# Optimization experiments

Hardware: AMD Instinct MI355X
Metric: run time of the kernel (lower is better)

Reference implementation:

```python
import jax, jax.numpy as jnp
import numpy as np

N_NODES = 100000
N_EDGES = 1600000
IN_CH = 128
HID = 256
OUT_CH = 128
N_GRAPHS = 2048


def setup_inputs() -> dict:
    key = jax.random.key(0)
    ks = jax.random.split(key, 12)
    x = jax.random.normal(ks[0], (N_NODES, IN_CH), dtype=jnp.float32)
    edge_index = jax.random.randint(ks[1], (2, N_EDGES), 0, N_NODES, dtype=jnp.int32)
    batch = jnp.sort(jax.random.randint(ks[2], (N_NODES,), 0, N_GRAPHS, dtype=jnp.int32))
    s = lambda k, shp, fan: jax.random.normal(k, shp, dtype=jnp.float32) / np.sqrt(fan)
    params = {
        # SAGEConv1: lin_l (applied to aggregated neighbors, has bias) and lin_r (root)
        "W1l": s(ks[3], (IN_CH, HID), IN_CH), "b1": jnp.zeros((HID,), jnp.float32),
        "W1r": s(ks[4], (IN_CH, HID), IN_CH),
        # SAGEConv2
        "W2l": s(ks[5], (HID, HID), HID), "b2": jnp.zeros((HID,), jnp.float32),
        "W2r": s(ks[6], (HID, HID), HID),
        # MLP head
        "W3": s(ks[7], (HID, HID), HID), "b3": jnp.zeros((HID,), jnp.float32),
        "W4": s(ks[8], (HID, OUT_CH), HID), "b4": jnp.zeros((OUT_CH,), jnp.float32),
    }
    return {"x": x, "edge_index": edge_index, "batch": batch, **params}


def _sage_conv(x, src, dst, Wl, bl, Wr, num_nodes):
    # PyG SAGEConv (aggr='mean'): out_i = Wl @ mean_{j->i} x_j + bl + Wr @ x_i
    agg = jax.ops.segment_sum(x[src], dst, num_segments=num_nodes)  # [N, C]
    cnt = jax.ops.segment_sum(jnp.ones((src.shape[0],), x.dtype), dst, num_segments=num_nodes)
    mean = agg / jnp.maximum(cnt, 1.0)[:, None]
    return mean @ Wl + bl + x @ Wr


def reference(x, edge_index, batch, W1l, b1, W1r, W2l, b2, W2r, W3, b3, W4, b4):
    src, dst = edge_index[0], edge_index[1]
    h = jax.nn.relu(_sage_conv(x, src, dst, W1l, b1, W1r, N_NODES))
    # dropout is identity in eval mode
    h = jax.nn.relu(_sage_conv(h, src, dst, W2l, b2, W2r, N_NODES))
    # global_mean_pool over graphs
    psum = jax.ops.segment_sum(h, batch, num_segments=N_GRAPHS)  # [G, HID]
    gcnt = jax.ops.segment_sum(jnp.ones((h.shape[0],), h.dtype), batch, num_segments=N_GRAPHS)
    pooled = psum / jnp.maximum(gcnt, 1.0)[:, None]
    # MLP head
    hidden = jax.nn.relu(pooled @ W3 + b3)
    return hidden @ W4 + b4  # [G, OUT_CH]
```

## Files before the change

kernel.cpp:

```cpp
#include <hip/hip_runtime.h>

#define N_NODES 100000
#define N_EDGES 1600000
#define IN_CH 128
#define HID 256
#define OUT_CH 128
#define N_GRAPHS 2048

#define NBUK 391
#define CHUNK 8192

typedef __attribute__((ext_vector_type(8))) short bf16x8;
typedef __attribute__((ext_vector_type(4))) float f32x4;
typedef __attribute__((ext_vector_type(2))) float f32x2;

__device__ inline unsigned short f2b(float f) {
    unsigned int u = __builtin_bit_cast(unsigned int, f);
    u = (u + 0x7FFF + ((u >> 16) & 1)) >> 16;
    return (unsigned short)u;
}
__device__ inline float b2f(unsigned short h) {
    unsigned int u = (unsigned int)h << 16;
    return __builtin_bit_cast(float, u);
}

#define GLOAD_LDS16(gsrc, ldst)                                                   \
    __builtin_amdgcn_global_load_lds(                                             \
        (const __attribute__((address_space(1))) void*)(gsrc),                    \
        (__attribute__((address_space(3))) void*)(ldst), 16, 0, 0)

#define SCAN_ITEMS 8
#define SCAN_TILE (256 * SCAN_ITEMS)

__global__ void scan1_k(const int* __restrict__ in, int* __restrict__ out,
                        int* __restrict__ bsums, int n) {
    __shared__ int wsum[4];
    int base = blockIdx.x * SCAN_TILE + (int)threadIdx.x * SCAN_ITEMS;
    int v[SCAN_ITEMS];
    int s = 0;
    #pragma unroll
    for (int i = 0; i < SCAN_ITEMS; ++i) {
        v[i] = (base + i < n) ? in[base + i] : 0;
        s += v[i];
    }
    int lane = threadIdx.x & 63, wid = threadIdx.x >> 6;
    int incl = s;
    #pragma unroll
    for (int off = 1; off < 64; off <<= 1) {
        int t = __shfl_up(incl, off, 64);
        if (lane >= off) incl += t;
    }
    if (lane == 63) wsum[wid] = incl;
    __syncthreads();
    int wprefix = 0;
    #pragma unroll
    for (int w = 0; w < 4; ++w)
        if (w < wid) wprefix += wsum[w];
    int run = wprefix + incl - s;
    #pragma unroll
    for (int i = 0; i < SCAN_ITEMS; ++i) {
        if (base + i < n) out[base + i] = run;
        run += v[i];
    }
    if (threadIdx.x == 255) bsums[blockIdx.x] = wprefix + incl;
}

__global__ void scan2_k(int* __restrict__ bsums, int nb, int* __restrict__ total) {
    __shared__ int wsum[4];
    int v = ((int)threadIdx.x < nb) ? bsums[threadIdx.x] : 0;
    int lane = threadIdx.x & 63, wid = threadIdx.x >> 6;
    int incl = v;
    #pragma unroll
    for (int off = 1; off < 64; off <<= 1) {
        int t = __shfl_up(incl, off, 64);
        if (lane >= off) incl += t;
    }
    if (lane == 63) wsum[wid] = incl;
    __syncthreads();
    int wprefix = 0;
    #pragma unroll
    for (int w = 0; w < 4; ++w)
        if (w < wid) wprefix += wsum[w];
    if ((int)threadIdx.x < nb) bsums[threadIdx.x] = wprefix + incl - v;
    if (threadIdx.x == 255) *total = wprefix + incl;
}

__global__ void bucket_count_k(const int* __restrict__ dst, int* __restrict__ bcnt, int E) {
    __shared__ int cnt[NBUK];
    int tid = threadIdx.x;
    for (int i = tid; i < NBUK; i += 256) cnt[i] = 0;
    __syncthreads();
    int e0 = blockIdx.x * CHUNK;
    int eend = min(e0 + CHUNK, E);
    for (int e = e0 + tid; e < eend; e += 256)
        atomicAdd(&cnt[dst[e] >> 8], 1);
    __syncthreads();
    for (int i = tid; i < NBUK; i += 256)
        if (cnt[i]) atomicAdd(&bcnt[i], cnt[i]);
}

__global__ void bin_scatter_k(const int* __restrict__ src, const int* __restrict__ dst,
                              const int* __restrict__ bbase, int* __restrict__ bcur,
                              uint2* __restrict__ staging, int E) {
    __shared__ int cnt[NBUK];
    __shared__ int gbase[NBUK];
    int tid = threadIdx.x;
    for (int i = tid; i < NBUK; i += 256) cnt[i] = 0;
    __syncthreads();
    int e0 = blockIdx.x * CHUNK;
    int eend = min(e0 + CHUNK, E);
    for (int e = e0 + tid; e < eend; e += 256)
        atomicAdd(&cnt[dst[e] >> 8], 1);
    __syncthreads();
    for (int i = tid; i < NBUK; i += 256) {
        int c = cnt[i];
        gbase[i] = c ? (bbase[i] + atomicAdd(&bcur[i], c)) : 0;
        cnt[i] = 0;
    }
    __syncthreads();
    for (int e = e0 + tid; e < eend; e += 256) {
        int d = dst[e];
        int b = d >> 8;
        int l = atomicAdd(&cnt[b], 1);
        uint2 p; p.x = (unsigned)src[e]; p.y = (unsigned)d;
        staging[(size_t)gbase[b] + l] = p;
    }
}

__global__ void csr_build_k(const uint2* __restrict__ staging, const int* __restrict__ bbase,
                            int* __restrict__ row_ofs, int* __restrict__ csr) {
    __shared__ int ldeg[256];
    __shared__ int lofs[256];
    __shared__ int wsum[4];
    int b = blockIdx.x, tid = threadIdx.x;
    int base = bbase[b];
    int cnt = bbase[b + 1] - base;
    ldeg[tid] = 0;
    __syncthreads();
    const uint2* sp = staging + base;
    for (int i = tid; i < cnt; i += 256)
        atomicAdd(&ldeg[sp[i].y & 255], 1);
    __syncthreads();
    int v = ldeg[tid];
    int lane = tid & 63, wid = tid >> 6;
    int incl = v;
    #pragma unroll
    for (int off = 1; off < 64; off <<= 1) {
        int t = __shfl_up(incl, off, 64);
        if (lane >= off) incl += t;
    }
    if (lane == 63) wsum[wid] = incl;
    __syncthreads();
    int wprefix = 0;
    #pragma unroll
    for (int w = 0; w < 4; ++w)
        if (w < wid) wprefix += wsum[w];
    int excl = wprefix + incl - v;
    lofs[tid] = excl;
    int node = b * 256 + tid;
    if (node < N_NODES) row_ofs[node] = base + excl;
    if (b == NBUK - 1 && tid == 0) row_ofs[N_NODES] = N_EDGES;
    ldeg[tid] = 0;
    __syncthreads();
    for (int i = tid; i < cnt; i += 256) {
        uint2 p = sp[i];
        int d = (int)p.y & 255;
        int pos = atomicAdd(&ldeg[d], 1);
        csr[base + lofs[d] + pos] = (int)p.x;
    }
}

__global__ void gofs_search_k(const int* __restrict__ batch, int* __restrict__ gofs,
                              int n, int G) {
    int g = blockIdx.x * blockDim.x + threadIdx.x;
    if (g > G) return;
    if (g == G) { gofs[G] = n; return; }
    int lo = 0, hi = n;
    while (lo < hi) {
        int mid = (lo + hi) >> 1;
        if (batch[mid] < g) lo = mid + 1; else hi = mid;
    }
    gofs[g] = lo;
}

__global__ void wt_concat_k(const float* __restrict__ Wl, const float* __restrict__ Wr,
                            unsigned short* __restrict__ out, int K1, int K2, int N) {
    int idx = blockIdx.x * blockDim.x + threadIdx.x;
    int KT = K1 + K2;
    if (idx >= N * KT) return;
    int n = idx / KT, k = idx % KT;
    float v = (k < K1) ? Wl[(size_t)k * N + n] : Wr[(size_t)(k - K1) * N + n];
    out[idx] = f2b(v);
}

__global__ void f2b8_k(const float* __restrict__ in, unsigned short* __restrict__ outb,
                       unsigned char* __restrict__ out8, size_t n8) {
    size_t i = (size_t)blockIdx.x * blockDim.x + threadIdx.x;
    if (i >= n8) return;
    float4 a = ((const float4*)in)[i * 2];
    float4 b = ((const float4*)in)[i * 2 + 1];
    unsigned short ob[8];
    ob[0] = f2b(a.x); ob[1] = f2b(a.y); ob[2] = f2b(a.z); ob[3] = f2b(a.w);
    ob[4] = f2b(b.x); ob[5] = f2b(b.y); ob[6] = f2b(b.z); ob[7] = f2b(b.w);
    ((uint4*)outb)[i] = *(const uint4*)ob;
    int w0 = 0, w1 = 0;
    w0 = __builtin_amdgcn_cvt_pk_fp8_f32(a.x, a.y, w0, false);
    w0 = __builtin_amdgcn_cvt_pk_fp8_f32(a.z, a.w, w0, true);
    w1 = __builtin_amdgcn_cvt_pk_fp8_f32(b.x, b.y, w1, false);
    w1 = __builtin_amdgcn_cvt_pk_fp8_f32(b.z, b.w, w1, true);
    uint2 o8; o8.x = (unsigned int)w0; o8.y = (unsigned int)w1;
    ((uint2*)out8)[i] = o8;
}

template <int C>
__global__ void agg_f8_k(const unsigned char* __restrict__ X8, const int* __restrict__ row_ofs,
                         const int* __restrict__ csr, unsigned short* __restrict__ out, int n) {
    constexpr int GL = C / 16;
    constexpr int NG = 64 / GL;
    int w = (int)((blockIdx.x * blockDim.x + threadIdx.x) >> 6);
    int lane = threadIdx.x & 63;
    if (w >= n) return;
    int g = lane / GL, il = lane % GL;
    int s = row_ofs[w], e = row_ofs[w + 1];
    float a[16];
    #pragma unroll
    for (int t = 0; t < 16; ++t) a[t] = 0.f;

    int j = s + g;
    for (; j + NG < e; j += 2 * NG) {
        int i0 = csr[j], i1 = csr[j + NG];
        uint4 r0 = *(const uint4*)&X8[(size_t)i0 * C + il * 16];
        uint4 r1 = *(const uint4*)&X8[(size_t)i1 * C + il * 16];
        const unsigned int* q0 = (const unsigned int*)&r0;
        const unsigned int* q1 = (const unsigned int*)&r1;
        #pragma unroll
        for (int t = 0; t < 4; ++t) {
            f32x2 lo = __builtin_amdgcn_cvt_pk_f32_fp8(q0[t], false);
            f32x2 hi = __builtin_amdgcn_cvt_pk_f32_fp8(q0[t], true);
            a[t * 4 + 0] += lo.x; a[t * 4 + 1] += lo.y;
            a[t * 4 + 2] += hi.x; a[t * 4 + 3] += hi.y;
        }
        #pragma unroll
        for (int t = 0; t < 4; ++t) {
            f32x2 lo = __builtin_amdgcn_cvt_pk_f32_fp8(q1[t], false);
            f32x2 hi = __builtin_amdgcn_cvt_pk_f32_fp8(q1[t], true);
            a[t * 4 + 0] += lo.x; a[t * 4 + 1] += lo.y;
            a[t * 4 + 2] += hi.x; a[t * 4 + 3] += hi.y;
        }
    }
    if (j < e) {
        int i0 = csr[j];
        uint4 r0 = *(const uint4*)&X8[(size_t)i0 * C + il * 16];
        const unsigned int* q0 = (const unsigned int*)&r0;
        #pragma unroll
        for (int t = 0; t < 4; ++t) {
            f32x2 lo = __builtin_amdgcn_cvt_pk_f32_fp8(q0[t], false);
            f32x2 hi = __builtin_amdgcn_cvt_pk_f32_fp8(q0[t], true);
            a[t * 4 + 0] += lo.x; a[t * 4 + 1] += lo.y;
            a[t * 4 + 2] += hi.x; a[t * 4 + 3] += hi.y;
        }
    }

    #pragma unroll
    for (int m = GL; m < 64; m <<= 1)
        #pragma unroll
        for (int t = 0; t < 16; ++t) a[t] += __shfl_xor(a[t], m, 64);

    if (g == 0) {
        float inv = 1.0f / (float)max(e - s, 1);
        uint4 o0, o1;
        unsigned short* p0 = (unsigned short*)&o0;
        unsigned short* p1 = (unsigned short*)&o1;
        #pragma unroll
        for (int t = 0; t < 8; ++t) p0[t] = f2b(a[t] * inv);
        #pragma unroll
        for (int t = 0; t < 8; ++t) p1[t] = f2b(a[8 + t] * inv);
        *(uint4*)&out[(size_t)w * C + il * 16] = o0;
        *(uint4*)&out[(size_t)w * C + il * 16 + 8] = o1;
    }
}

__global__ void pool_mean_k(const unsigned short* __restrict__ H, const int* __restrict__ gofs,
                            float* __restrict__ pooled, int G) {
    int g = (int)((blockIdx.x * blockDim.x + threadIdx.x) >> 6);
    int lane = threadIdx.x & 63;
    if (g >= G) return;
    int s = gofs[g], e = gofs[g + 1];
    float a0 = 0.f, a1 = 0.f, a2 = 0.f, a3 = 0.f;
    for (int r = s; r < e; ++r) {
        ushort4 t = ((const ushort4*)(H + (size_t)r * HID))[lane];
        a0 += b2f(t.x); a1 += b2f(t.y); a2 += b2f(t.z); a3 += b2f(t.w);
    }
    float inv = 1.0f / (float)max(e - s, 1);
    float4 o; o.x = a0 * inv; o.y = a1 * inv; o.z = a2 * inv; o.w = a3 * inv;
    ((float4*)(pooled + (size_t)g * HID))[lane] = o;
}

__launch_bounds__(256)
__global__ void mfma_gemm_k(const unsigned short* __restrict__ A1, int K1,
                            const unsigned short* __restrict__ A2, int K2,
                            const unsigned short* __restrict__ Bt,
                            const float* __restrict__ bias, int M, int Nfull,
                            void* __restrict__ Cptr, unsigned char* __restrict__ f8out,
                            int c_bf16, int do_relu) {
    __shared__ short ldsA[3 * 4096];
    __shared__ short ldsB[3 * 4096];
    int tid = threadIdx.x, lane = tid & 63;
    int wid = tid >> 6, wm = wid >> 1, wn = wid & 1;
    int row0 = blockIdx.x * 128, col0 = blockIdx.y * 128;
    int q = lane >> 4, l15 = lane & 15;
    int KT = K1 + K2;
    int nk = KT / 32;

    int rr = tid >> 2;
    int c8 = ((tid & 3) ^ (rr & 3)) * 8;
    int dof = wid * 512;

    auto stage = [&](int t, short* bA, short* bB) {
        int kt = t * 32;
        const unsigned short* Asrc; int kk, Ks;
        if (kt < K1) { Asrc = A1; kk = kt; Ks = K1; }
        else         { Asrc = A2; kk = kt - K1; Ks = K2; }
        #pragma unroll
        for (int h = 0; h < 2; ++h) {
            int r = h * 64 + rr;
            int gr = min(row0 + r, M - 1);
            GLOAD_LDS16(Asrc + (size_t)gr * Ks + kk + c8, bA + h * 2048 + dof);
            GLOAD_LDS16(Bt + (size_t)(col0 + r) * KT + kt + c8, bB + h * 2048 + dof);
        }
    };

    f32x4 acc[4][4] = {};

    stage(0, ldsA, ldsB);
    stage(1, ldsA + 4096, ldsB + 4096);
    stage(2, ldsA + 8192, ldsB + 8192);

    int bi = 0;
    for (int t = 0; t < nk; ++t) {
        if (t + 2 < nk)      asm volatile("s_waitcnt vmcnt(8)" ::: "memory");
        else if (t + 1 < nk) asm volatile("s_waitcnt vmcnt(4)" ::: "memory");
        else                 asm volatile("s_waitcnt vmcnt(0)" ::: "memory");
        asm volatile("s_barrier" ::: "memory");

        short* bA = ldsA + bi * 4096;
        short* bB = ldsB + bi * 4096;
        bf16x8 af[4], bfr[4];
        #pragma unroll
        for (int i = 0; i < 4; ++i) {
            int r = wm * 64 + i * 16 + l15;
            af[i] = *(const bf16x8*)&bA[r * 32 + (q ^ (r & 3)) * 8];
        }
        #pragma unroll
        for (int j = 0; j < 4; ++j) {
            int r = wn * 64 + j * 16 + l15;
            bfr[j] = *(const bf16x8*)&bB[r * 32 + (q ^ (r & 3)) * 8];
        }
        #pragma unroll
        for (int i = 0; i < 4; ++i)
            #pragma unroll
            for (int j = 0; j < 4; ++j)
                acc[i][j] = __builtin_amdgcn_mfma_f32_16x16x32_bf16(af[i], bfr[j], acc[i][j], 0, 0, 0);

        asm volatile("s_barrier" ::: "memory");
        if (t + 3 < nk) stage(t + 3, bA, bB);
        bi = (bi == 2) ? 0 : bi + 1;
    }

    #pragma unroll
    for (int i = 0; i < 4; ++i) {
        #pragma unroll
        for (int reg = 0; reg < 4; ++reg) {
            int r = row0 + wm * 64 + i * 16 + q * 4 + reg;
            if (r < M) {
                #pragma unroll
                for (int j = 0; j < 4; ++j) {
                    int cc = col0 + wn * 64 + j * 16 + l15;
                    float v = acc[i][j][reg] + bias[cc];
                    if (do_relu) v = fmaxf(v, 0.f);
                    if (c_bf16) ((unsigned short*)Cptr)[(size_t)r * Nfull + cc] = f2b(v);
                    else        ((float*)Cptr)[(size_t)r * Nfull + cc] = v;
                    if (f8out) {
                        int w8 = __builtin_amdgcn_cvt_pk_fp8_f32(v, v, 0, false);
                        f8out[(size_t)r * Nfull + cc] = (unsigned char)(w8 & 0xFF);
                    }
                }
            }
        }
    }
}

#define BM_ 64
#define BK_ 16

template <int BN_>
__launch_bounds__(256)
__global__ void gemm2_k(const float* __restrict__ A1, const float* __restrict__ B1, int K1,
                        const float* __restrict__ bias, float* __restrict__ C,
                        int M, int N, int do_relu) {
    constexpr int TCOLS = BN_ / 8;
    constexpr int TROWS = 256 / TCOLS;
    constexpr int TM = BM_ / TROWS;
    __shared__ float As[BK_][BM_ + 4];
    __shared__ float Bs[BK_][BN_ + 4];
    int tid = threadIdx.x;
    int row0 = blockIdx.x * BM_;
    int col0 = blockIdx.y * BN_;
    int tx = tid % TCOLS, ty = tid / TCOLS;

    float acc[TM][8];
    #pragma unroll
    for (int i = 0; i < TM; ++i)
        #pragma unroll
        for (int j = 0; j < 8; ++j) acc[i][j] = 0.f;

    int ar = tid >> 2;
    int ak = (tid & 3) * 4;

    for (int kt = 0; kt < K1; kt += BK_) {
        {
            int r = row0 + ar;
            int rc = min(r, M - 1);
            float4 v = *(const float4*)(A1 + (size_t)rc * K1 + kt + ak);
            As[ak + 0][ar] = v.x;
            As[ak + 1][ar] = v.y;
            As[ak + 2][ar] = v.z;
            As[ak + 3][ar] = v.w;
        }
        {
            #pragma unroll
            for (int h = 0; h < BN_ / 64; ++h) {
                int idx = h * 256 + tid;
                int kr = idx / (BN_ / 4);
                int c4 = idx % (BN_ / 4);
                float4 v = *(const float4*)(B1 + (size_t)(kt + kr) * N + col0 + c4 * 4);
                *(float4*)&Bs[kr][c4 * 4] = v;
            }
        }
        __syncthreads();

        #pragma unroll
        for (int k = 0; k < BK_; ++k) {
            float a[TM], b[8];
            #pragma unroll
            for (int v = 0; v < TM / 4; ++v)
                *(float4*)&a[v * 4] = *(const float4*)&As[k][ty * TM + v * 4];
            *(float4*)&b[0] = *(const float4*)&Bs[k][tx * 8];
            *(float4*)&b[4] = *(const float4*)&Bs[k][tx * 8 + 4];
            #pragma unroll
            for (int i = 0; i < TM; ++i)
                #pragma unroll
                for (int j = 0; j < 8; ++j) acc[i][j] = fmaf(a[i], b[j], acc[i][j]);
        }
        __syncthreads();
    }

    float bv[8];
    #pragma unroll
    for (int j = 0; j < 8; ++j) bv[j] = bias[col0 + tx * 8 + j];
    #pragma unroll
    for (int i = 0; i < TM; ++i) {
        int r = row0 + ty * TM + i;
        if (r < M) {
            float* cp = C + (size_t)r * N + col0 + tx * 8;
            float o[8];
            #pragma unroll
            for (int j = 0; j < 8; ++j) {
                float v = acc[i][j] + bv[j];
                o[j] = do_relu ? fmaxf(v, 0.f) : v;
            }
            *(float4*)(cp + 0) = *(float4*)&o[0];
            *(float4*)(cp + 4) = *(float4*)&o[4];
        }
    }
}

extern "C" void kernel_launch(void* const* d_in, const int* in_sizes, int n_in,
                              void* d_out, int out_size, void* d_ws, size_t ws_size,
                              hipStream_t stream) {
    const float* x    = (const float*)d_in[0];
    const int*   ei   = (const int*)d_in[1];
    const int*   batch= (const int*)d_in[2];
    const float* W1l  = (const float*)d_in[3];
    const float* b1   = (const float*)d_in[4];
    const float* W1r  = (const float*)d_in[5];
    const float* W2l  = (const float*)d_in[6];
    const float* b2   = (const float*)d_in[7];
    const float* W2r  = (const float*)d_in[8];
    const float* W3   = (const float*)d_in[9];
    const float* b3   = (const float*)d_in[10];
    const float* W4   = (const float*)d_in[11];
    const float* b4   = (const float*)d_in[12];
    float* out = (float*)d_out;

    const int N = N_NODES, E = N_EDGES, G = N_GRAPHS;
    const int* src = ei;
    const int* dst = ei + E;

    char* ws = (char*)d_ws;
    size_t off = 0;
    auto alloc = [&](size_t bytes) -> char* {
        off = (off + 255) & ~(size_t)255;
        char* p = ws + off;
        off += bytes;
        return p;
    };
    int* bcnt    = (int*)alloc((size_t)NBUK * 4);
    int* bcur    = (int*)alloc((size_t)NBUK * 4);
    size_t zero_span = (size_t)((char*)(bcur + NBUK) - (char*)bcnt);
    int* bbase   = (int*)alloc((size_t)(NBUK + 1) * 4);
    int* bsums   = (int*)alloc(256 * 4);
    int* row_ofs = (int*)alloc((size_t)(N + 1) * 4);
    int* gofs    = (int*)alloc((size_t)(G + 1) * 4);
    uint2* staging = (uint2*)alloc((size_t)E * 8);
    int* csr     = (int*)alloc((size_t)E * 4);
    unsigned short* xb    = (unsigned short*)alloc((size_t)N * IN_CH * 2);
    unsigned short* mean1 = (unsigned short*)alloc((size_t)N * IN_CH * 2);
    unsigned short* h1    = (unsigned short*)alloc((size_t)N * HID * 2);
    unsigned short* mean2 = (unsigned short*)alloc((size_t)N * HID * 2);
    unsigned short* h2    = xb;
    unsigned char*  x8    = (unsigned char*)alloc((size_t)N * IN_CH);
    unsigned char*  h1f8  = (unsigned char*)alloc((size_t)N * HID);
    unsigned short* W1T   = (unsigned short*)alloc((size_t)HID * (IN_CH + IN_CH) * 2);
    unsigned short* W2T   = (unsigned short*)alloc((size_t)HID * (HID + HID) * 2);
    float* pooled = (float*)alloc((size_t)G * HID * 4);
    float* hidden = (float*)alloc((size_t)G * HID * 4);
    (void)ws_size;

    hipMemsetAsync(bcnt, 0, zero_span, stream);

    const int EB = (E + CHUNK - 1) / CHUNK;
    bucket_count_k<<<EB, 256, 0, stream>>>(dst, bcnt, E);
    scan1_k<<<1, 256, 0, stream>>>(bcnt, bbase, bsums, NBUK);
    scan2_k<<<1, 256, 0, stream>>>(bsums, 1, bbase + NBUK);
    bin_scatter_k<<<EB, 256, 0, stream>>>(src, dst, bbase, bcur, staging, E);
    csr_build_k<<<NBUK, 256, 0, stream>>>(staging, bbase, row_ofs, csr);

    gofs_search_k<<<(G + 256) / 256, 256, 0, stream>>>(batch, gofs, N, G);

    wt_concat_k<<<(HID * 2 * IN_CH + 255) / 256, 256, 0, stream>>>(W1l, W1r, W1T, IN_CH, IN_CH, HID);
    wt_concat_k<<<(HID * 2 * HID + 255) / 256, 256, 0, stream>>>(W2l, W2r, W2T, HID, HID, HID);
    f2b8_k<<<(int)(((size_t)N * IN_CH / 8 + 255) / 256), 256, 0, stream>>>(
        x, xb, x8, (size_t)N * IN_CH / 8);

    const int MB = (N + 127) / 128;

    agg_f8_k<IN_CH><<<(N + 3) / 4, 256, 0, stream>>>(x8, row_ofs, csr, mean1, N);
    mfma_gemm_k<<<dim3(MB, HID / 128), 256, 0, stream>>>(
        mean1, IN_CH, xb, IN_CH, W1T, b1, N, HID, h1, h1f8, 1, 1);

    agg_f8_k<HID><<<(N + 3) / 4, 256, 0, stream>>>(h1f8, row_ofs, csr, mean2, N);
    mfma_gemm_k<<<dim3(MB, HID / 128), 256, 0, stream>>>(
        mean2, HID, h1, HID, W2T, b2, N, HID, h2, nullptr, 1, 1);

    pool_mean_k<<<(G + 3) / 4, 256, 0, stream>>>(h2, gofs, pooled, G);

    gemm2_k<HID><<<dim3(G / BM_, 1), 256, 0, stream>>>(
        pooled, W3, HID, b3, hidden, G, HID, 1);
    gemm2_k<OUT_CH><<<dim3(G / BM_, 1), 256, 0, stream>>>(
        hidden, W4, HID, b4, out, G, OUT_CH, 0);
}
```

Before: 551.7 us.

## Widen MFMA GEMM tile to 128x256 with 8 waves and split-stage pipeline

```diff
diff --git a/kernel.cpp b/kernel.cpp
--- a/kernel.cpp
+++ b/kernel.cpp
@@ -296,75 +296,114 @@
     ((float4*)(pooled + (size_t)g * HID))[lane] = o;
 }
 
-__launch_bounds__(256)
+__launch_bounds__(512)
 __global__ void mfma_gemm_k(const unsigned short* __restrict__ A1, int K1,
                             const unsigned short* __restrict__ A2, int K2,
                             const unsigned short* __restrict__ Bt,
                             const float* __restrict__ bias, int M, int Nfull,
                             void* __restrict__ Cptr, unsigned char* __restrict__ f8out,
                             int c_bf16, int do_relu) {
-    __shared__ short ldsA[3 * 4096];
-    __shared__ short ldsB[3 * 4096];
+    __shared__ short lds[3 * 24576];
     int tid = threadIdx.x, lane = tid & 63;
-    int wid = tid >> 6, wm = wid >> 1, wn = wid & 1;
-    int row0 = blockIdx.x * 128, col0 = blockIdx.y * 128;
+    int wid = tid >> 6, wm = wid >> 2, wn = wid & 3;
+    int row0 = blockIdx.x * 128, col0 = blockIdx.y * 256;
     int q = lane >> 4, l15 = lane & 15;
     int KT = K1 + K2;
-    int nk = KT / 32;
-
-    int rr = tid >> 2;
-    int c8 = ((tid & 3) ^ (rr & 3)) * 8;
-    int dof = wid * 512;
-
-    auto stage = [&](int t, short* bA, short* bB) {
-        int kt = t * 32;
+    int nk = KT / 64;
+
+    int lr = lane >> 3;
+    int cg = (lane & 7) ^ lr;
+
+    auto stagep = [&](int t, int part) {
+        int kt = t * 64;
         const unsigned short* Asrc; int kk, Ks;
         if (kt < K1) { Asrc = A1; kk = kt; Ks = K1; }
         else         { Asrc = A2; kk = kt - K1; Ks = K2; }
-        #pragma unroll
-        for (int h = 0; h < 2; ++h) {
-            int r = h * 64 + rr;
-            int gr = min(row0 + r, M - 1);
-            GLOAD_LDS16(Asrc + (size_t)gr * Ks + kk + c8, bA + h * 2048 + dof);
-            GLOAD_LDS16(Bt + (size_t)(col0 + r) * KT + kt + c8, bB + h * 2048 + dof);
+        short* bufA = lds + (t % 3) * 24576;
+        short* bufB = bufA + 8192;
+        if (part == 0) {
+            #pragma unroll
+            for (int h = 0; h < 2; ++h) {
+                int rl = h * 64 + wid * 8 + lr;
+                int gr = min(row0 + rl, M - 1);
+                GLOAD_LDS16(Asrc + (size_t)gr * Ks + kk + cg * 8,
+                            bufA + (h * 64 + wid * 8) * 64);
+            }
+            {
+                int rl = wid * 8 + lr;
+                GLOAD_LDS16(Bt + (size_t)(col0 + rl) * KT + kt + cg * 8,
+                            bufB + (wid * 8) * 64);
+            }
+        } else {
+            #pragma unroll
+            for (int h = 1; h < 4; ++h) {
+                int rl = h * 64 + wid * 8 + lr;
+                GLOAD_LDS16(Bt + (size_t)(col0 + rl) * KT + kt + cg * 8,
+                            bufB + (h * 64 + wid * 8) * 64);
+            }
         }
     };
 
     f32x4 acc[4][4] = {};
 
-    stage(0, ldsA, ldsB);
-    stage(1, ldsA + 4096, ldsB + 4096);
-    stage(2, ldsA + 8192, ldsB + 8192);
-
-    int bi = 0;
+    stagep(0, 0); stagep(0, 1);
+    stagep(1, 0); stagep(1, 1);
+
     for (int t = 0; t < nk; ++t) {
-        if (t + 2 < nk)      asm volatile("s_waitcnt vmcnt(8)" ::: "memory");
-        else if (t + 1 < nk) asm volatile("s_waitcnt vmcnt(4)" ::: "memory");
-        else                 asm volatile("s_waitcnt vmcnt(0)" ::: "memory");
+        if (t + 1 < nk) asm volatile("s_waitcnt vmcnt(6)" ::: "memory");
+        else            asm volatile("s_waitcnt vmcnt(0)" ::: "memory");
         asm volatile("s_barrier" ::: "memory");
-
-        short* bA = ldsA + bi * 4096;
-        short* bB = ldsB + bi * 4096;
-        bf16x8 af[4], bfr[4];
-        #pragma unroll
-        for (int i = 0; i < 4; ++i) {
-            int r = wm * 64 + i * 16 + l15;
-            af[i] = *(const bf16x8*)&bA[r * 32 + (q ^ (r & 3)) * 8];
-        }
-        #pragma unroll
-        for (int j = 0; j < 4; ++j) {
-            int r = wn * 64 + j * 16 + l15;
-            bfr[j] = *(const bf16x8*)&bB[r * 32 + (q ^ (r & 3)) * 8];
-        }
-        #pragma unroll
-        for (int i = 0; i < 4; ++i)
+        const short* bufA = lds + (t % 3) * 24576;
+        const short* bufB = bufA + 8192;
+
+        bf16x8 bfr[4][2], af[2][2];
+        #pragma unroll
+        for (int j = 0; j < 4; ++j)
+            #pragma unroll
+            for (int s = 0; s < 2; ++s) {
+                int r = wn * 64 + j * 16 + l15;
+                bfr[j][s] = *(const bf16x8*)&bufB[r * 64 + ((s * 4 + q) ^ (r & 7)) * 8];
+            }
+        #pragma unroll
+        for (int i = 0; i < 2; ++i)
+            #pragma unroll
+            for (int s = 0; s < 2; ++s) {
+                int r = wm * 64 + i * 16 + l15;
+                af[i][s] = *(const bf16x8*)&bufA[r * 64 + ((s * 4 + q) ^ (r & 7)) * 8];
+            }
+        if (t + 2 < nk) stagep(t + 2, 0);
+        __builtin_amdgcn_s_setprio(1);
+        #pragma unroll
+        for (int i = 0; i < 2; ++i)
             #pragma unroll
             for (int j = 0; j < 4; ++j)
-                acc[i][j] = __builtin_amdgcn_mfma_f32_16x16x32_bf16(af[i], bfr[j], acc[i][j], 0, 0, 0);
-
+                #pragma unroll
+                for (int s = 0; s < 2; ++s)
+                    acc[i][j] = __builtin_amdgcn_mfma_f32_16x16x32_bf16(
+                        af[i][s], bfr[j][s], acc[i][j], 0, 0, 0);
+        __builtin_amdgcn_s_setprio(0);
         asm volatile("s_barrier" ::: "memory");
-        if (t + 3 < nk) stage(t + 3, bA, bB);
-        bi = (bi == 2) ? 0 : bi + 1;
+
+        bf16x8 af2[2][2];
+        #pragma unroll
+        for (int i = 0; i < 2; ++i)
+            #pragma unroll
+            for (int s = 0; s < 2; ++s) {
+                int r = wm * 64 + (i + 2) * 16 + l15;
+                af2[i][s] = *(const bf16x8*)&bufA[r * 64 + ((s * 4 + q) ^ (r & 7)) * 8];
+            }
+        if (t + 2 < nk) stagep(t + 2, 1);
+        __builtin_amdgcn_s_setprio(1);
+        #pragma unroll
+        for (int i = 0; i < 2; ++i)
+            #pragma unroll
+            for (int j = 0; j < 4; ++j)
+                #pragma unroll
+                for (int s = 0; s < 2; ++s)
+                    acc[i + 2][j] = __builtin_amdgcn_mfma_f32_16x16x32_bf16(
+                        af2[i][s], bfr[j][s], acc[i + 2][j], 0, 0, 0);
+        __builtin_amdgcn_s_setprio(0);
+        asm volatile("s_barrier" ::: "memory");
     }
 
     #pragma unroll
@@ -543,14 +582,14 @@
     f2b8_k<<<(int)(((size_t)N * IN_CH / 8 + 255) / 256), 256, 0, stream>>>(
         x, xb, x8, (size_t)N * IN_CH / 8);
 
-    const int MB = (N + 127) / 128;
+    const int MB128 = (N + 127) / 128;
 
     agg_f8_k<IN_CH><<<(N + 3) / 4, 256, 0, stream>>>(x8, row_ofs, csr, mean1, N);
-    mfma_gemm_k<<<dim3(MB, HID / 128), 256, 0, stream>>>(
+    mfma_gemm_k<<<dim3(MB128, HID / 256), 512, 0, stream>>>(
         mean1, IN_CH, xb, IN_CH, W1T, b1, N, HID, h1, h1f8, 1, 1);
 
     agg_f8_k<HID><<<(N + 3) / 4, 256, 0, stream>>>(h1f8, row_ofs, csr, mean2, N);
-    mfma_gemm_k<<<dim3(MB, HID / 128), 256, 0, stream>>>(
+    mfma_gemm_k<<<dim3(MB128, HID / 256), 512, 0, stream>>>(
         mean2, HID, h1, HID, W2T, b2, N, HID, h2, nullptr, 1, 1);
 
     pool_mean_k<<<(G + 3) / 4, 256, 0, stream>>>(h2, gofs, pooled, G);
```

Result: slower. 564.9 us (+2.4%).
